# Kernel tuning notes

Hardware: AMD Instinct MI355X
Metric: run time of the kernel (lower is better)

The kernel has to match this reference:

```python
import jax, jax.numpy as jnp
import numpy as np

B, L, D, H = 2, 4096, 512, 8
HD = D // H  # head_dim = 64


def setup_inputs() -> dict:
    key = jax.random.key(0)
    ks = jax.random.split(key, 5)
    s = 0.02
    return {
        "x": jax.random.normal(ks[0], (B, L, D), dtype=jnp.float32),
        "w_qkv": jax.random.normal(ks[1], (D, 3 * D), dtype=jnp.float32) * s,
        "b_qkv": jax.random.normal(ks[2], (3 * D,), dtype=jnp.float32) * s,
        "w_o": jax.random.normal(ks[3], (D, D), dtype=jnp.float32) * s,
        "b_o": jax.random.normal(ks[4], (D,), dtype=jnp.float32) * s,
    }


def reference(x, w_qkv, b_qkv, w_o, b_o):
    b, l, _ = x.shape
    # QKV projection, then split heads: [B, L, 3D] -> [B, H, L, 3*HD]
    qkv = x @ w_qkv + b_qkv
    qkv = qkv.reshape(b, l, H, 3 * HD).transpose(0, 2, 1, 3)
    q, k, v = jnp.split(qkv, 3, axis=-1)  # each [B, H, L, HD]
    scale = 1.0 / jnp.sqrt(jnp.asarray(HD, dtype=q.dtype))
    # full score matrix [B, H, L, L], softmax in float32 (matches .float() cast)
    scores = jnp.einsum('bhld,bhsd->bhls', q, k) * scale
    attn = jax.nn.softmax(scores.astype(jnp.float32), axis=-1).astype(q.dtype)
    values = jnp.einsum('bhls,bhsd->bhld', attn, v)  # [B, H, L, HD]
    values = values.transpose(0, 2, 1, 3).reshape(b, l, D)
    return values @ w_o + b_o
```

## Files before the change

kernel.cpp:

```cpp
#include <hip/hip_runtime.h>


#define B_  2
#define L_  4096
#define D_  512
#define H_  8
#define HD_ 64
#define BH_ (B_*H_)
#define M_  (B_*L_)
#define QKVN (3*D_)
#define HEADSZ (BH_*L_*HD_)

typedef unsigned short ushort;
typedef unsigned int uint;
typedef __bf16 bf16x8 __attribute__((ext_vector_type(8)));
typedef float  f32x4  __attribute__((ext_vector_type(4)));
typedef float  f32x16 __attribute__((ext_vector_type(16)));

typedef const __attribute__((address_space(1))) void g_void;
typedef __attribute__((address_space(3))) void l_void;

#define C2_ 0.18033688011112042f

#if __has_builtin(__builtin_amdgcn_exp2f)
#define FEXP2(x) __builtin_amdgcn_exp2f(x)
#else
#define FEXP2(x) exp2f(x)
#endif

__device__ __forceinline__ ushort f2bf(float f) {
    __bf16 h = (__bf16)f;
    return __builtin_bit_cast(ushort, h);
}

__device__ __forceinline__ uint pack2(float lo, float hi) {
    return (uint)f2bf(lo) | ((uint)f2bf(hi) << 16);
}

__global__ __launch_bounds__(256)
void prep_k(const float* __restrict__ x, ushort* __restrict__ xb,
            const float* __restrict__ wq, ushort* __restrict__ wtq,
            const float* __restrict__ wo, ushort* __restrict__ wto)
{
    int bid = blockIdx.x, tid = threadIdx.x;
    if (bid < 4096) {
        int idx = bid * 256 + tid;
        float4 v = ((const float4*)x)[idx];
        ushort4 o; o.x = f2bf(v.x); o.y = f2bf(v.y); o.z = f2bf(v.z); o.w = f2bf(v.w);
        ((ushort4*)xb)[idx] = o;
    } else if (bid < 7168) {
        int idx = (bid - 4096) * 256 + tid;
        int c = idx / D_, r = idx % D_;
        wtq[idx] = f2bf(wq[r * QKVN + c]);
    } else {
        int idx = (bid - 7168) * 256 + tid;
        int c = idx / D_, r = idx % D_;
        wto[idx] = f2bf(wo[r * D_ + c]);
    }
}

#define TP 66
__global__ __launch_bounds__(256)
void transpose_v(const ushort* __restrict__ V, ushort* __restrict__ VT) {
    __shared__ ushort T[64 * TP];
    const int tid = threadIdx.x;
    const int bh = blockIdx.y;
    const int l0 = blockIdx.x * 64;
    const int base = bh * (L_ * HD_);
    #pragma unroll
    for (int i = 0; i < 2; i++) {
        int c = i * 256 + tid;
        int l = c >> 3, dc = (c & 7) * 8;
        uint4 v = *(const uint4*)&V[base + (l0 + l) * HD_ + dc];
        uint* p = (uint*)&T[l * TP + dc];
        p[0] = v.x; p[1] = v.y; p[2] = v.z; p[3] = v.w;
    }
    __syncthreads();
    #pragma unroll
    for (int p = 0; p < 2; p++) {
        int c = p * 256 + tid;
        int d = c >> 3, lb = c & 7;
        ushort tmp[8];
        #pragma unroll
        for (int j = 0; j < 8; j++) tmp[j] = T[(lb * 8 + j) * TP + d];
        *(uint4*)&VT[base + d * L_ + l0 + lb * 8] = *(uint4*)tmp;
    }
}

__global__ __launch_bounds__(256)
void gemm_bt(const ushort* __restrict__ A, const ushort* __restrict__ Bt,
             const float* __restrict__ bias, void* __restrict__ out,
             int M, int N, int K, int mode)
{
    __shared__ ushort As[128 * 32];
    __shared__ ushort Bs[128 * 32];

    const int tid  = threadIdx.x;
    const int lane = tid & 63;
    const int wid  = tid >> 6;
    const int wm   = wid >> 1, wn = wid & 1;
    const int lr   = lane & 15;
    const int quad = lane >> 4;
    const int tm = blockIdx.x, tn = blockIdx.y;

    f32x4 acc[4][4] = {};
    const int arow = tm * 128;
    const int brow = tn * 128;

    for (int k0 = 0; k0 < K; k0 += 32) {
        #pragma unroll
        for (int i = 0; i < 2; i++) {
            int c   = i * 256 + tid;
            int row = c >> 2;
            int kk  = (c & 3) * 8;
            __builtin_amdgcn_global_load_lds(
                (g_void*)&A[(size_t)(arow + row) * K + k0 + kk],
                (l_void*)&As[c * 8], 16, 0, 0);
            __builtin_amdgcn_global_load_lds(
                (g_void*)&Bt[(size_t)(brow + row) * K + k0 + kk],
                (l_void*)&Bs[c * 8], 16, 0, 0);
        }
        __syncthreads();

        bf16x8 af[4], bfr[4];
        #pragma unroll
        for (int t = 0; t < 4; t++) {
            af [t] = *(const bf16x8*)&As[(wm * 64 + t * 16 + lr) * 32 + quad * 8];
            bfr[t] = *(const bf16x8*)&Bs[(wn * 64 + t * 16 + lr) * 32 + quad * 8];
        }
        #pragma unroll
        for (int mt = 0; mt < 4; mt++)
            #pragma unroll
            for (int nt = 0; nt < 4; nt++)
                acc[mt][nt] = __builtin_amdgcn_mfma_f32_16x16x32_bf16(
                    af[mt], bfr[nt], acc[mt][nt], 0, 0, 0);
        __syncthreads();
    }

    #pragma unroll
    for (int nt = 0; nt < 4; nt++) {
        int col = tn * 128 + wn * 64 + nt * 16 + lr;
        float bv = bias[col];
        #pragma unroll
        for (int mt = 0; mt < 4; mt++) {
            #pragma unroll
            for (int r = 0; r < 4; r++) {
                int row = tm * 128 + wm * 64 + mt * 16 + quad * 4 + r;
                float v = acc[mt][nt][r] + bv;
                if (mode == 0) {
                    ((float*)out)[(size_t)row * N + col] = v;
                } else {
                    int d = col & 63;
                    int g = col >> 6;
                    int which = g % 3;
                    int h = g / 3;
                    int b = row >> 12;
                    int l = row & (L_ - 1);
                    if (which == 0) v *= C2_;
                    ((ushort*)out)[which * HEADSZ + (((b * H_ + h) * L_ + l) * HD_) + d]
                        = f2bf(v);
                }
            }
        }
    }
}

__global__ __launch_bounds__(256)
void attn_k(const ushort* __restrict__ Q, const ushort* __restrict__ K,
            const ushort* __restrict__ VT, ushort* __restrict__ O)
{
    __shared__ __align__(16) ushort Ksm[2][64 * 64];
    __shared__ __align__(16) ushort Vsm[4][64 * 64];

    const int tid  = threadIdx.x;
    const int lane = tid & 63;
    const int wid  = tid >> 6;
    const int l31  = lane & 31;
    const int hi   = lane >> 5;

    const int wg  = blockIdx.x;
    const int xcd = wg & 7, sl = wg >> 3;
    const int bh  = (xcd << 1) | (sl >> 5);
    const int q0  = (sl & 31) * 128;
    const size_t base = (size_t)bh * (L_ * HD_);

    const int sr0 = tid >> 3,        sr1 = (tid + 256) >> 3;
    const int sc0 = ((tid & 7) ^ (sr0 & 7)) * 8;
    const int sc1 = ((tid & 7) ^ (sr1 & 7)) * 8;
    const ushort* Kg0 = K  + base + sr0 * HD_ + sc0;
    const ushort* Kg1 = K  + base + sr1 * HD_ + sc1;
    const ushort* Vg0 = VT + base + (size_t)sr0 * L_ + sc0;
    const ushort* Vg1 = VT + base + (size_t)sr1 * L_ + sc1;

    bf16x8 qf[4];
    {
        const ushort* qp = Q + base + (size_t)(q0 + wid * 32 + l31) * HD_ + hi * 8;
        #pragma unroll
        for (int ks = 0; ks < 4; ks++) qf[ks] = *(const bf16x8*)(qp + ks * 16);
    }

    const int swz = (l31 & 7) << 4;
    int cbe[4];
    #pragma unroll
    for (int ks = 0; ks < 4; ks++) cbe[ks] = ((ks * 32 + hi * 16) ^ swz) >> 1;
    const int kr0 = l31 * 64, kr1 = (32 + l31) * 64;

    const f32x16 Z = {};
    bf16x8 onesB;
    #pragma unroll
    for (int i = 0; i < 8; i++) onesB[i] = (__bf16)1.0f;

    f32x16 o0 = {}, o1 = {}, l_acc = {};
    f32x16 sEA, sEB, sOA, sOB;

    auto STAGE = [&](int tt) {
        const size_t ko = (size_t)tt * 64 * HD_;
        const int    vo = tt * 64;
        ushort* kb = &Ksm[tt & 1][0];
        ushort* vb = &Vsm[tt & 3][0];
        __builtin_amdgcn_global_load_lds((g_void*)(Kg0 + ko), (l_void*)(kb + tid * 8),        16, 0, 0);
        __builtin_amdgcn_global_load_lds((g_void*)(Kg1 + ko), (l_void*)(kb + tid * 8 + 2048), 16, 0, 0);
        __builtin_amdgcn_global_load_lds((g_void*)(Vg0 + vo), (l_void*)(vb + tid * 8),        16, 0, 0);
        __builtin_amdgcn_global_load_lds((g_void*)(Vg1 + vo), (l_void*)(vb + tid * 8 + 2048), 16, 0, 0);
    };

    auto QK = [&](int tt, f32x16& SA, f32x16& SB) {
        const ushort* kb = &Ksm[tt & 1][0];
        {
            bf16x8 k0 = *(const bf16x8*)&kb[kr0 + cbe[0]];
            bf16x8 k1 = *(const bf16x8*)&kb[kr1 + cbe[0]];
            SA = __builtin_amdgcn_mfma_f32_32x32x16_bf16(k0, qf[0], Z, 0, 0, 0);
            SB = __builtin_amdgcn_mfma_f32_32x32x16_bf16(k1, qf[0], Z, 0, 0, 0);
        }
        #pragma unroll
        for (int ks = 1; ks < 4; ks++) {
            bf16x8 k0 = *(const bf16x8*)&kb[kr0 + cbe[ks]];
            bf16x8 k1 = *(const bf16x8*)&kb[kr1 + cbe[ks]];
            SA = __builtin_amdgcn_mfma_f32_32x32x16_bf16(k0, qf[ks], SA, 0, 0, 0);
            SB = __builtin_amdgcn_mfma_f32_32x32x16_bf16(k1, qf[ks], SB, 0, 0, 0);
        }
    };

    auto SMPV = [&](int tp, f32x16& SA, f32x16& SB) {
        const ushort* vb = &Vsm[tp & 3][0];
        #pragma unroll
        for (int i = 0; i < 16; i++) { SA[i] = FEXP2(SA[i]); SB[i] = FEXP2(SB[i]); }
        #pragma unroll
        for (int ks = 0; ks < 4; ks++) {
            const f32x16& P = (ks >> 1) ? SB : SA;
            const int r0 = 8 * (ks & 1);
            uint a0 = pack2(P[r0 + 0], P[r0 + 1]);
            uint a1 = pack2(P[r0 + 2], P[r0 + 3]);
            uint b0 = pack2(P[r0 + 4], P[r0 + 5]);
            uint b1 = pack2(P[r0 + 6], P[r0 + 7]);
            asm("v_permlane32_swap_b32 %0, %1" : "+v"(a0), "+v"(b0));
            asm("v_permlane32_swap_b32 %0, %1" : "+v"(a1), "+v"(b1));
            uint4 w; w.x = a0; w.y = a1; w.z = b0; w.w = b1;
            bf16x8 pa = __builtin_bit_cast(bf16x8, w);
            bf16x8 v0 = *(const bf16x8*)&vb[kr0 + cbe[ks]];
            bf16x8 v1 = *(const bf16x8*)&vb[kr1 + cbe[ks]];
            o0 = __builtin_amdgcn_mfma_f32_32x32x16_bf16(pa, v0, o0, 0, 0, 0);
            o1 = __builtin_amdgcn_mfma_f32_32x32x16_bf16(pa, v1, o1, 0, 0, 0);
            l_acc = __builtin_amdgcn_mfma_f32_32x32x16_bf16(pa, onesB, l_acc, 0, 0, 0);
        }
    };

    STAGE(0);

    for (int t = 0; t < L_ / 64; t += 2) {
        __syncthreads();
        STAGE(t + 1);
        QK(t, sEA, sEB);
        if (t > 0) SMPV(t - 1, sOA, sOB);
        __syncthreads();
        if (t + 2 < L_ / 64) STAGE(t + 2);
        QK(t + 1, sOA, sOB);
        SMPV(t, sEA, sEB);
    }
    SMPV(L_ / 64 - 1, sOA, sOB);

    const int b = bh >> 3, h = bh & 7;
    #pragma unroll
    for (int r = 0; r < 16; r++) {
        const int qrl = (r & 3) + 8 * (r >> 2) + 4 * hi;
        const float inv = 1.0f / l_acc[r];
        const size_t row = (size_t)(b * L_ + q0 + wid * 32 + qrl) * D_ + h * HD_ + l31;
        O[row]      = f2bf(o0[r] * inv);
        O[row + 32] = f2bf(o1[r] * inv);
    }
}

extern "C" void kernel_launch(void* const* d_in, const int* in_sizes, int n_in,
                              void* d_out, int out_size, void* d_ws, size_t ws_size,
                              hipStream_t stream)
{
    const float* x     = (const float*)d_in[0];
    const float* w_qkv = (const float*)d_in[1];
    const float* b_qkv = (const float*)d_in[2];
    const float* w_o   = (const float*)d_in[3];
    const float* b_o   = (const float*)d_in[4];

    char* ws = (char*)d_ws;
    size_t o = 0;
    ushort* xb   = (ushort*)(ws + o); o += (size_t)M_ * D_ * 2;
    ushort* qkv  = (ushort*)(ws + o); o += (size_t)3 * HEADSZ * 2;
    ushort* attn = (ushort*)(ws + o); o += (size_t)M_ * D_ * 2;
    ushort* wtq  = (ushort*)(ws + o); o += (size_t)QKVN * D_ * 2;
    ushort* wto  = (ushort*)(ws + o);
    ushort* vt   = xb;

    hipLaunchKernelGGL(prep_k, dim3(8192), dim3(256), 0, stream,
                       x, xb, w_qkv, wtq, w_o, wto);
    hipLaunchKernelGGL(gemm_bt, dim3(M_ / 128, QKVN / 128), dim3(256), 0, stream,
                       xb, wtq, b_qkv, (void*)qkv, M_, QKVN, D_, 1);
    hipLaunchKernelGGL(transpose_v, dim3(L_ / 64, BH_), dim3(256), 0, stream,
                       qkv + 2 * HEADSZ, vt);
    hipLaunchKernelGGL(attn_k, dim3(512), dim3(256), 0, stream,
                       qkv, qkv + HEADSZ, vt, attn);
    hipLaunchKernelGGL(gemm_bt, dim3(M_ / 128, D_ / 128), dim3(256), 0, stream,
                       attn, wto, b_o, d_out, M_, D_, D_, 0);
}
```

Before: 211.3 us.

## Double-buffer GEMM LDS tiles and use narrower N tile for output projection

The GEMM kernel now keeps two LDS buffers and issues the global-to-LDS loads for the next K step before computing on the current one. This removes the second barrier per iteration and overlaps memory latency with MFMA work. The kernel is also templated on the N tile width, and the output projection uses 128x64 tiles so it launches twice as many blocks for the narrow 512-column GEMM. The cost is double the LDS footprint per block. Relying on a single barrier per step also depends on global_load_lds writes into the other buffer not racing with reads of the current one.

```diff
diff --git a/kernel.cpp b/kernel.cpp
--- a/kernel.cpp
+++ b/kernel.cpp
@@ -87,27 +87,34 @@
     }
 }
 
+template<int BN>
 __global__ __launch_bounds__(256)
 void gemm_bt(const ushort* __restrict__ A, const ushort* __restrict__ Bt,
              const float* __restrict__ bias, void* __restrict__ out,
              int M, int N, int K, int mode)
 {
-    __shared__ ushort As[128 * 32];
-    __shared__ ushort Bs[128 * 32];
+    constexpr int MT = (BN == 128) ? 4 : 2;
+    constexpr int BL = BN / 64;
+    __shared__ ushort As[2][128 * 32];
+    __shared__ ushort Bs[2][BN * 32];
 
     const int tid  = threadIdx.x;
     const int lane = tid & 63;
     const int wid  = tid >> 6;
-    const int wm   = wid >> 1, wn = wid & 1;
+    const int wm   = (BN == 128) ? (wid >> 1) : wid;
+    const int wn   = (BN == 128) ? (wid & 1) : 0;
     const int lr   = lane & 15;
     const int quad = lane >> 4;
     const int tm = blockIdx.x, tn = blockIdx.y;
 
-    f32x4 acc[4][4] = {};
+    f32x4 acc[MT][4] = {};
     const int arow = tm * 128;
-    const int brow = tn * 128;
-
-    for (int k0 = 0; k0 < K; k0 += 32) {
+    const int brow = tn * BN;
+
+    auto STAGE = [&](int t) {
+        const int k0 = t * 32;
+        ushort* as = &As[t & 1][0];
+        ushort* bs = &Bs[t & 1][0];
         #pragma unroll
         for (int i = 0; i < 2; i++) {
             int c   = i * 256 + tid;
@@ -115,37 +122,51 @@
             int kk  = (c & 3) * 8;
             __builtin_amdgcn_global_load_lds(
                 (g_void*)&A[(size_t)(arow + row) * K + k0 + kk],
-                (l_void*)&As[c * 8], 16, 0, 0);
+                (l_void*)&as[c * 8], 16, 0, 0);
+        }
+        #pragma unroll
+        for (int i = 0; i < BL; i++) {
+            int c   = i * 256 + tid;
+            int row = c >> 2;
+            int kk  = (c & 3) * 8;
             __builtin_amdgcn_global_load_lds(
                 (g_void*)&Bt[(size_t)(brow + row) * K + k0 + kk],
-                (l_void*)&Bs[c * 8], 16, 0, 0);
-        }
+                (l_void*)&bs[c * 8], 16, 0, 0);
+        }
+    };
+
+    const int NK = K / 32;
+    STAGE(0);
+    for (int t = 0; t < NK; t++) {
         __syncthreads();
-
-        bf16x8 af[4], bfr[4];
-        #pragma unroll
-        for (int t = 0; t < 4; t++) {
-            af [t] = *(const bf16x8*)&As[(wm * 64 + t * 16 + lr) * 32 + quad * 8];
-            bfr[t] = *(const bf16x8*)&Bs[(wn * 64 + t * 16 + lr) * 32 + quad * 8];
-        }
-        #pragma unroll
-        for (int mt = 0; mt < 4; mt++)
+        if (t + 1 < NK) STAGE(t + 1);
+        const ushort* as = &As[t & 1][0];
+        const ushort* bs = &Bs[t & 1][0];
+
+        bf16x8 af[MT], bfr[4];
+        #pragma unroll
+        for (int mt = 0; mt < MT; mt++)
+            af[mt] = *(const bf16x8*)&as[(wm * (MT * 16) + mt * 16 + lr) * 32 + quad * 8];
+        #pragma unroll
+        for (int nt = 0; nt < 4; nt++)
+            bfr[nt] = *(const bf16x8*)&bs[(wn * 64 + nt * 16 + lr) * 32 + quad * 8];
+        #pragma unroll
+        for (int mt = 0; mt < MT; mt++)
             #pragma unroll
             for (int nt = 0; nt < 4; nt++)
                 acc[mt][nt] = __builtin_amdgcn_mfma_f32_16x16x32_bf16(
                     af[mt], bfr[nt], acc[mt][nt], 0, 0, 0);
-        __syncthreads();
     }
 
     #pragma unroll
     for (int nt = 0; nt < 4; nt++) {
-        int col = tn * 128 + wn * 64 + nt * 16 + lr;
+        int col = tn * BN + wn * 64 + nt * 16 + lr;
         float bv = bias[col];
         #pragma unroll
-        for (int mt = 0; mt < 4; mt++) {
+        for (int mt = 0; mt < MT; mt++) {
             #pragma unroll
             for (int r = 0; r < 4; r++) {
-                int row = tm * 128 + wm * 64 + mt * 16 + quad * 4 + r;
+                int row = tm * 128 + wm * (MT * 16) + mt * 16 + quad * 4 + r;
                 float v = acc[mt][nt][r] + bv;
                 if (mode == 0) {
                     ((float*)out)[(size_t)row * N + col] = v;
@@ -311,12 +332,12 @@
 
     hipLaunchKernelGGL(prep_k, dim3(8192), dim3(256), 0, stream,
                        x, xb, w_qkv, wtq, w_o, wto);
-    hipLaunchKernelGGL(gemm_bt, dim3(M_ / 128, QKVN / 128), dim3(256), 0, stream,
+    hipLaunchKernelGGL((gemm_bt<128>), dim3(M_ / 128, QKVN / 128), dim3(256), 0, stream,
                        xb, wtq, b_qkv, (void*)qkv, M_, QKVN, D_, 1);
     hipLaunchKernelGGL(transpose_v, dim3(L_ / 64, BH_), dim3(256), 0, stream,
                        qkv + 2 * HEADSZ, vt);
     hipLaunchKernelGGL(attn_k, dim3(512), dim3(256), 0, stream,
                        qkv, qkv + HEADSZ, vt, attn);
-    hipLaunchKernelGGL(gemm_bt, dim3(M_ / 128, D_ / 128), dim3(256), 0, stream,
+    hipLaunchKernelGGL((gemm_bt<64>), dim3(M_ / 128, D_ / 64), dim3(256), 0, stream,
                        attn, wto, b_o, d_out, M_, D_, D_, 0);
 }
```

Measured after the change: 209.7 us. No clear change (-0.8%).
